# Kernel optimization log

Hardware: AMD Instinct MI355X
Metric: run time of the kernel (lower is better)

Reference implementation:

```python
import jax, jax.numpy as jnp
import numpy as np

B, I, H, N_STEPS = 256, 1024, 1024, 128


def setup_inputs() -> dict:
    key = jax.random.key(0)
    ks = jax.random.split(key, 12)
    s_ih = 1.0 / np.sqrt(H)
    u = lambda k, shp: jax.random.uniform(k, shp, jnp.float32, -s_ih, s_ih)
    return {
        "x": jax.random.normal(ks[0], (B, 1, I), jnp.float32),
        "n": N_STEPS,
        "w_ih_f": u(ks[1], (3 * H, I)),
        "w_hh_f": u(ks[2], (3 * H, H)),
        "b_ih_f": u(ks[3], (3 * H,)),
        "b_hh_f": u(ks[4], (3 * H,)),
        "w_ih_b": u(ks[5], (3 * H, I)),
        "w_hh_b": u(ks[6], (3 * H, H)),
        "b_ih_b": u(ks[7], (3 * H,)),
        "b_hh_b": u(ks[8], (3 * H,)),
        "w_out": u(ks[9], (1, 2 * H)),
        "b_out": u(ks[10], (1,)),
    }


def _gru_step(h, gi, w_hh, b_hh):
    # gi: precomputed input gates (B, 3H); h: (B, H)
    gh = h @ w_hh.T + b_hh
    gi_r, gi_z, gi_n = jnp.split(gi, 3, axis=-1)
    gh_r, gh_z, gh_n = jnp.split(gh, 3, axis=-1)
    r = jax.nn.sigmoid(gi_r + gh_r)
    z = jax.nn.sigmoid(gi_z + gh_z)
    ng = jnp.tanh(gi_n + r * gh_n)
    return (1.0 - z) * ng + z * h


def reference(x, n, w_ih_f, w_hh_f, b_ih_f, b_hh_f,
              w_ih_b, w_hh_b, b_ih_b, b_hh_b, w_out, b_out):
    x0 = x[:, 0, :]  # (B, I); cur_x never changes in the original loop
    # input-side gates are constant across steps (same x fed each time)
    gi_f = x0 @ w_ih_f.T + b_ih_f  # (B, 3H)
    gi_b = x0 @ w_ih_b.T + b_ih_b
    h0 = jnp.zeros((x.shape[0], w_hh_f.shape[1]), x.dtype)

    def step(carry, _):
        hf, hb = carry
        hf = _gru_step(hf, gi_f, w_hh_f, b_hh_f)
        hb = _gru_step(hb, gi_b, w_hh_b, b_hh_b)
        out = jnp.concatenate([hf, hb], axis=-1) @ w_out.T + b_out  # (B, 1)
        return (hf, hb), out

    _, outs = jax.lax.scan(step, (h0, h0), None, length=n)
    return jnp.transpose(outs, (1, 0, 2))  # (B, n, 1)
```

## Files before the change

kernel.cpp:

```cpp
#include <hip/hip_runtime.h>
#include <hip/hip_bf16.h>

typedef __attribute__((ext_vector_type(8))) __bf16 bf16x8;
typedef __attribute__((ext_vector_type(16))) float f32x16;
typedef __attribute__((ext_vector_type(4)))  float f32x4;

#define NB 256
#define HD 1024
#define G3 3072
#define NT 128

static const size_t OFF_WHH  = 0;
static const size_t OFF_WIH  = OFF_WHH + (size_t)2*G3*HD*2;
static const size_t OFF_X16  = OFF_WIH + (size_t)2*G3*HD*2;
static const size_t OFF_FLG  = OFF_X16 + (size_t)NB*HD*2;
static const size_t OFF_H16  = OFF_FLG + 65536;
static const size_t OFF_PART = OFF_H16 + (size_t)4*NB*HD*2;

__global__ __launch_bounds__(256) void prep_kernel(
    const float* __restrict__ x,    const float* __restrict__ wihf,
    const float* __restrict__ whhf, const float* __restrict__ wihb,
    const float* __restrict__ whhb, char* __restrict__ ws)
{
  size_t i = (size_t)blockIdx.x*256 + threadIdx.x;
  __hip_bfloat16* whh = (__hip_bfloat16*)(ws+OFF_WHH);
  __hip_bfloat16* wih = (__hip_bfloat16*)(ws+OFF_WIH);
  __hip_bfloat16* x16 = (__hip_bfloat16*)(ws+OFF_X16);
  __hip_bfloat16* h16 = (__hip_bfloat16*)(ws+OFF_H16);
  if (i < 16384) ((unsigned*)(ws+OFF_FLG))[i] = 0u;
  if (i < (size_t)G3*HD) {
    whh[i]                 = __float2bfloat16(whhf[i]);
    whh[(size_t)G3*HD + i] = __float2bfloat16(whhb[i]);
    wih[i]                 = __float2bfloat16(wihf[i]);
    wih[(size_t)G3*HD + i] = __float2bfloat16(wihb[i]);
  }
  if (i < (size_t)NB*HD)   x16[i] = __float2bfloat16(x[i]);
  if (i < (size_t)2*NB*HD) h16[i]  = __float2bfloat16(0.f);
}

__device__ inline f32x4 gload_cc(const void* p){
  f32x4 r;
  asm volatile("global_load_dwordx4 %0, %1, off sc0 sc1" : "=v"(r) : "v"(p) : "memory");
  return r;
}
__device__ inline void gstore_cc(void* p, f32x4 v){
  asm volatile("global_store_dwordx4 %0, %1, off sc0 sc1" :: "v"(p), "v"(v) : "memory");
}

__global__ __launch_bounds__(256,1)
void gru_persist(char* __restrict__ ws,
                 const float* __restrict__ bihf, const float* __restrict__ bhhf,
                 const float* __restrict__ bihb, const float* __restrict__ bhhb,
                 const float* __restrict__ wout)
{
  const int bid = blockIdx.x;
  const int g8  = bid & 7;
  const int d   = g8 >> 2;
  const int rt  = g8 & 3;
  const int jt  = bid >> 3;
  const int tid = threadIdx.x;
  const int q   = tid >> 6;
  const int l   = tid & 63;
  const int lrow = l & 31;
  const int lh   = l >> 5;
  const int erow = l & 15;
  const int ec   = l >> 4;
  const int r0 = rt*64, j0 = jt*32;

  const __hip_bfloat16* Wih = (const __hip_bfloat16*)(ws+OFF_WIH) + (size_t)d*G3*HD;
  const __hip_bfloat16* Whh = (const __hip_bfloat16*)(ws+OFF_WHH) + (size_t)d*G3*HD;
  const __hip_bfloat16* X16 = (const __hip_bfloat16*)(ws+OFF_X16);
  __hip_bfloat16* H16 = (__hip_bfloat16*)(ws+OFF_H16);
  unsigned* flg = (unsigned*)(ws+OFF_FLG);
  float* part = (float*)(ws+OFF_PART);

  __shared__ float red[4][64][100];

  const int kbase = (q*32 + lh)*8;

  bf16x8 B[3][16];
  auto loadB = [&](const __hip_bfloat16* Wsrc){
    #pragma unroll
    for (int g=0; g<3; ++g){
      const __hip_bfloat16* p0 = Wsrc + (size_t)(g*1024 + j0 + lrow)*HD + kbase;
      #pragma unroll
      for (int ks=0; ks<16; ++ks) B[g][ks] = *(const bf16x8*)(p0 + ks*16);
    }
  };

  f32x16 acc[2][3];
  auto gemm_cc = [&](const __hip_bfloat16* Asrc){
    #pragma unroll
    for (int mi=0;mi<2;++mi)
      #pragma unroll
      for (int g=0;g<3;++g)
        #pragma unroll
        for (int e=0;e<16;++e) acc[mi][g][e] = 0.f;
    const __hip_bfloat16* pa0 = Asrc + (size_t)(r0 + lrow)*HD + kbase;
    const __hip_bfloat16* pa1 = pa0 + 32*HD;
    f32x4 A0a[4], A0b[4], A1a[4], A1b[4];
    #pragma unroll
    for (int ks=0; ks<4; ++ks){ A0a[ks]=gload_cc(pa0+ks*16);      A1a[ks]=gload_cc(pa1+ks*16); }
    #pragma unroll
    for (int ks=0; ks<4; ++ks){ A0b[ks]=gload_cc(pa0+(4+ks)*16);  A1b[ks]=gload_cc(pa1+(4+ks)*16); }

    asm volatile("s_waitcnt vmcnt(8)" ::: "memory");
    __builtin_amdgcn_sched_barrier(0);
    #pragma unroll
    for (int ks=0; ks<4; ++ks){
      bf16x8 a0 = __builtin_bit_cast(bf16x8, A0a[ks]);
      bf16x8 a1 = __builtin_bit_cast(bf16x8, A1a[ks]);
      #pragma unroll
      for (int g=0; g<3; ++g){
        acc[0][g] = __builtin_amdgcn_mfma_f32_32x32x16_bf16(a0, B[g][ks], acc[0][g],0,0,0);
        acc[1][g] = __builtin_amdgcn_mfma_f32_32x32x16_bf16(a1, B[g][ks], acc[1][g],0,0,0);
      }
    }
    #pragma unroll
    for (int ks=0; ks<4; ++ks){ A0a[ks]=gload_cc(pa0+(8+ks)*16);  A1a[ks]=gload_cc(pa1+(8+ks)*16); }

    asm volatile("s_waitcnt vmcnt(8)" ::: "memory");
    __builtin_amdgcn_sched_barrier(0);
    #pragma unroll
    for (int ks=0; ks<4; ++ks){
      bf16x8 a0 = __builtin_bit_cast(bf16x8, A0b[ks]);
      bf16x8 a1 = __builtin_bit_cast(bf16x8, A1b[ks]);
      #pragma unroll
      for (int g=0; g<3; ++g){
        acc[0][g] = __builtin_amdgcn_mfma_f32_32x32x16_bf16(a0, B[g][4+ks], acc[0][g],0,0,0);
        acc[1][g] = __builtin_amdgcn_mfma_f32_32x32x16_bf16(a1, B[g][4+ks], acc[1][g],0,0,0);
      }
    }
    #pragma unroll
    for (int ks=0; ks<4; ++ks){ A0b[ks]=gload_cc(pa0+(12+ks)*16); A1b[ks]=gload_cc(pa1+(12+ks)*16); }

    asm volatile("s_waitcnt vmcnt(8)" ::: "memory");
    __builtin_amdgcn_sched_barrier(0);
    #pragma unroll
    for (int ks=0; ks<4; ++ks){
      bf16x8 a0 = __builtin_bit_cast(bf16x8, A0a[ks]);
      bf16x8 a1 = __builtin_bit_cast(bf16x8, A1a[ks]);
      #pragma unroll
      for (int g=0; g<3; ++g){
        acc[0][g] = __builtin_amdgcn_mfma_f32_32x32x16_bf16(a0, B[g][8+ks], acc[0][g],0,0,0);
        acc[1][g] = __builtin_amdgcn_mfma_f32_32x32x16_bf16(a1, B[g][8+ks], acc[1][g],0,0,0);
      }
    }

    asm volatile("s_waitcnt vmcnt(0)" ::: "memory");
    __builtin_amdgcn_sched_barrier(0);
    #pragma unroll
    for (int ks=0; ks<4; ++ks){
      bf16x8 a0 = __builtin_bit_cast(bf16x8, A0b[ks]);
      bf16x8 a1 = __builtin_bit_cast(bf16x8, A1b[ks]);
      #pragma unroll
      for (int g=0; g<3; ++g){
        acc[0][g] = __builtin_amdgcn_mfma_f32_32x32x16_bf16(a0, B[g][12+ks], acc[0][g],0,0,0);
        acc[1][g] = __builtin_amdgcn_mfma_f32_32x32x16_bf16(a1, B[g][12+ks], acc[1][g],0,0,0);
      }
    }
  };

  float val[3][8];
  auto reduce = [&](){
    #pragma unroll
    for (int mi=0;mi<2;++mi)
      #pragma unroll
      for (int g=0;g<3;++g)
        #pragma unroll
        for (int e=0;e<16;++e){
          int rl = mi*32 + (e&3) + 8*(e>>2) + 4*lh;
          red[q][rl][g*32 + lrow] = acc[mi][g][e];
        }
    __syncthreads();
    #pragma unroll
    for (int g=0; g<3; ++g){
      #pragma unroll
      for (int c=0;c<8;++c) val[g][c] = 0.f;
      #pragma unroll
      for (int qq=0; qq<4; ++qq){
        const float* base = &red[qq][q*16+erow][g*32 + ec*8];
        float4 v0 = *(const float4*)base;
        float4 v1 = *(const float4*)(base+4);
        val[g][0]+=v0.x; val[g][1]+=v0.y; val[g][2]+=v0.z; val[g][3]+=v0.w;
        val[g][4]+=v1.x; val[g][5]+=v1.y; val[g][6]+=v1.z; val[g][7]+=v1.w;
      }
    }
    __syncthreads();
  };

  loadB(Wih);
  gemm_cc(X16);
  reduce();
  const float* bih = d ? bihb : bihf;
  const float* bhh = d ? bhhb : bhhf;
  const int cg = j0 + ec*8;
  float gir[8], giz[8], gin[8], bhn[8], wo8[8], h[8];
  #pragma unroll
  for (int c=0;c<8;++c){
    gir[c] = val[0][c] + bih[cg+c]      + bhh[cg+c];
    giz[c] = val[1][c] + bih[1024+cg+c] + bhh[1024+cg+c];
    gin[c] = val[2][c] + bih[2048+cg+c];
    bhn[c] = bhh[2048+cg+c];
    wo8[c] = wout[d*HD + cg + c];
    h[c]   = 0.f;
  }

  loadB(Whh);
  const int myrow = r0 + q*16 + erow;
  const size_t hplane = (size_t)2*NB*HD;

  for (int t=0; t<NT; ++t){
    if (t){
      const unsigned tgt = (unsigned)t;
      unsigned* fp = flg + (size_t)(g8*32 + q*8 + (l & 7))*32;
      for(;;){
        unsigned v = (l < 8) ? __hip_atomic_load(fp, __ATOMIC_RELAXED, __HIP_MEMORY_SCOPE_AGENT) : tgt;
        if (__all((int)(v >= tgt))) break;
        __builtin_amdgcn_s_sleep(1);
      }
    }

    const __hip_bfloat16* hs = H16 + (size_t)(t&1)*hplane + (size_t)d*NB*HD;
    gemm_cc(hs);
    reduce();
    bf16x8 hv;
    float pp = 0.f;
    #pragma unroll
    for (int c=0;c<8;++c){
      float rr = 1.f/(1.f+__expf(-(gir[c]+val[0][c])));
      float zz = 1.f/(1.f+__expf(-(giz[c]+val[1][c])));
      float ar = gin[c] + rr*(val[2][c]+bhn[c]);
      float ng = 1.f - 2.f/(1.f + __expf(2.f*ar));
      h[c] = (1.f-zz)*ng + zz*h[c];
      hv[c] = (__bf16)h[c];
      pp += h[c]*wo8[c];
    }
    __hip_bfloat16* hd = H16 + (size_t)((t+1)&1)*hplane + (size_t)d*NB*HD;
    gstore_cc(hd + (size_t)myrow*HD + cg, __builtin_bit_cast(f32x4, hv));
    pp += __shfl_xor(pp, 16, 64);
    pp += __shfl_xor(pp, 32, 64);
    if (l < 16) part[((size_t)myrow*NT + t)*64 + d*32 + jt] = pp;

    asm volatile("s_waitcnt vmcnt(0)" ::: "memory");
    __syncthreads();
    if (t+1 < NT && tid == 0) atomicAdd(flg + (size_t)(g8*32 + jt)*32, 1u);
  }
}

__global__ __launch_bounds__(256) void finalize_kernel(
    const char* __restrict__ ws, const float* __restrict__ bout,
    float* __restrict__ out)
{
  int widx = blockIdx.x*4 + (threadIdx.x>>6);
  int lane = threadIdx.x & 63;
  const float* part = (const float*)(ws+OFF_PART);
  float v = part[(size_t)widx*64 + lane];
  #pragma unroll
  for (int m=1;m<64;m<<=1) v += __shfl_xor(v, m, 64);
  if (lane==0) out[widx] = v + bout[0];
}

extern "C" void kernel_launch(void* const* d_in, const int* in_sizes, int n_in,
                              void* d_out, int out_size, void* d_ws, size_t ws_size,
                              hipStream_t stream)
{
  const float* x    = (const float*)d_in[0];
  const float* wihf = (const float*)d_in[2];
  const float* whhf = (const float*)d_in[3];
  const float* bihf = (const float*)d_in[4];
  const float* bhhf = (const float*)d_in[5];
  const float* wihb = (const float*)d_in[6];
  const float* whhb = (const float*)d_in[7];
  const float* bihb = (const float*)d_in[8];
  const float* bhhb = (const float*)d_in[9];
  const float* wout = (const float*)d_in[10];
  const float* bout = (const float*)d_in[11];
  char* ws = (char*)d_ws;
  float* out = (float*)d_out;

  prep_kernel<<<12288, 256, 0, stream>>>(x, wihf, whhf, wihb, whhb, ws);
  gru_persist<<<256, 256, 0, stream>>>(ws, bihf, bhhf, bihb, bhhb, wout);
  finalize_kernel<<<8192, 256, 0, stream>>>(ws, bout, out);
}
```

Before: 1.059 ms.

## Use L2-scoped h loads/stores when all communicating blocks share an XCC

Each block records its XCC id at runtime, and the blocks that exchange hidden state (same g8 group) check whether they all sit on the same XCC. If they do, the per-step h exchange uses loads and stores with L2-level coherence instead of system-coherent sc0 sc1 accesses, aiming to cut the latency of the recurrent GEMM's operand fetch. Otherwise it falls back to the old path. It adds a one-time global census with spinning, and the fast path relies on block-to-XCC placement, which the hardware may not provide.

```diff
diff --git a/kernel.cpp b/kernel.cpp
--- a/kernel.cpp
+++ b/kernel.cpp
@@ -14,6 +14,8 @@
 static const size_t OFF_WIH  = OFF_WHH + (size_t)2*G3*HD*2;
 static const size_t OFF_X16  = OFF_WIH + (size_t)2*G3*HD*2;
 static const size_t OFF_FLG  = OFF_X16 + (size_t)NB*HD*2;
+static const size_t OFF_XTAB = OFF_FLG + 32768;
+static const size_t OFF_XCNT = OFF_XTAB + 1024;
 static const size_t OFF_H16  = OFF_FLG + 65536;
 static const size_t OFF_PART = OFF_H16 + (size_t)4*NB*HD*2;
 
@@ -46,6 +48,75 @@
 __device__ inline void gstore_cc(void* p, f32x4 v){
   asm volatile("global_store_dwordx4 %0, %1, off sc0 sc1" :: "v"(p), "v"(v) : "memory");
 }
+__device__ inline f32x4 gload_l2(const void* p){
+  f32x4 r;
+  asm volatile("global_load_dwordx4 %0, %1, off sc0" : "=v"(r) : "v"(p) : "memory");
+  return r;
+}
+__device__ inline void gstore_l2(void* p, f32x4 v){
+  asm volatile("global_store_dwordx4 %0, %1, off" :: "v"(p), "v"(v) : "memory");
+}
+__device__ inline unsigned gload_u32_cc(const void* p){
+  unsigned r;
+  asm volatile("global_load_dword %0, %1, off sc0 sc1" : "=v"(r) : "v"(p) : "memory");
+  return r;
+}
+__device__ inline void gstore_u32_cc(void* p, unsigned v){
+  asm volatile("global_store_dword %0, %1, off sc0 sc1" :: "v"(p), "v"(v) : "memory");
+}
+
+#define GEMM_BODY(ASRC, LOADH) { \
+    _Pragma("unroll") for (int mi=0;mi<2;++mi) \
+      _Pragma("unroll") for (int g=0;g<3;++g) \
+        _Pragma("unroll") for (int e=0;e<16;++e) acc[mi][g][e] = 0.f; \
+    const __hip_bfloat16* pa0 = (ASRC) + (size_t)(r0 + lrow)*HD + kbase; \
+    const __hip_bfloat16* pa1 = pa0 + 32*HD; \
+    f32x4 A0a[4], A0b[4], A1a[4], A1b[4]; \
+    _Pragma("unroll") for (int ks=0; ks<4; ++ks){ A0a[ks]=LOADH(pa0+ks*16);      A1a[ks]=LOADH(pa1+ks*16); } \
+    _Pragma("unroll") for (int ks=0; ks<4; ++ks){ A0b[ks]=LOADH(pa0+(4+ks)*16);  A1b[ks]=LOADH(pa1+(4+ks)*16); } \
+    asm volatile("s_waitcnt vmcnt(8)" ::: "memory"); \
+    __builtin_amdgcn_sched_barrier(0); \
+    _Pragma("unroll") for (int ks=0; ks<4; ++ks){ \
+      bf16x8 a0 = __builtin_bit_cast(bf16x8, A0a[ks]); \
+      bf16x8 a1 = __builtin_bit_cast(bf16x8, A1a[ks]); \
+      _Pragma("unroll") for (int g=0; g<3; ++g){ \
+        acc[0][g] = __builtin_amdgcn_mfma_f32_32x32x16_bf16(a0, B[g][ks], acc[0][g],0,0,0); \
+        acc[1][g] = __builtin_amdgcn_mfma_f32_32x32x16_bf16(a1, B[g][ks], acc[1][g],0,0,0); \
+      } \
+    } \
+    _Pragma("unroll") for (int ks=0; ks<4; ++ks){ A0a[ks]=LOADH(pa0+(8+ks)*16);  A1a[ks]=LOADH(pa1+(8+ks)*16); } \
+    asm volatile("s_waitcnt vmcnt(8)" ::: "memory"); \
+    __builtin_amdgcn_sched_barrier(0); \
+    _Pragma("unroll") for (int ks=0; ks<4; ++ks){ \
+      bf16x8 a0 = __builtin_bit_cast(bf16x8, A0b[ks]); \
+      bf16x8 a1 = __builtin_bit_cast(bf16x8, A1b[ks]); \
+      _Pragma("unroll") for (int g=0; g<3; ++g){ \
+        acc[0][g] = __builtin_amdgcn_mfma_f32_32x32x16_bf16(a0, B[g][4+ks], acc[0][g],0,0,0); \
+        acc[1][g] = __builtin_amdgcn_mfma_f32_32x32x16_bf16(a1, B[g][4+ks], acc[1][g],0,0,0); \
+      } \
+    } \
+    _Pragma("unroll") for (int ks=0; ks<4; ++ks){ A0b[ks]=LOADH(pa0+(12+ks)*16); A1b[ks]=LOADH(pa1+(12+ks)*16); } \
+    asm volatile("s_waitcnt vmcnt(8)" ::: "memory"); \
+    __builtin_amdgcn_sched_barrier(0); \
+    _Pragma("unroll") for (int ks=0; ks<4; ++ks){ \
+      bf16x8 a0 = __builtin_bit_cast(bf16x8, A0a[ks]); \
+      bf16x8 a1 = __builtin_bit_cast(bf16x8, A1a[ks]); \
+      _Pragma("unroll") for (int g=0; g<3; ++g){ \
+        acc[0][g] = __builtin_amdgcn_mfma_f32_32x32x16_bf16(a0, B[g][8+ks], acc[0][g],0,0,0); \
+        acc[1][g] = __builtin_amdgcn_mfma_f32_32x32x16_bf16(a1, B[g][8+ks], acc[1][g],0,0,0); \
+      } \
+    } \
+    asm volatile("s_waitcnt vmcnt(0)" ::: "memory"); \
+    __builtin_amdgcn_sched_barrier(0); \
+    _Pragma("unroll") for (int ks=0; ks<4; ++ks){ \
+      bf16x8 a0 = __builtin_bit_cast(bf16x8, A0b[ks]); \
+      bf16x8 a1 = __builtin_bit_cast(bf16x8, A1b[ks]); \
+      _Pragma("unroll") for (int g=0; g<3; ++g){ \
+        acc[0][g] = __builtin_amdgcn_mfma_f32_32x32x16_bf16(a0, B[g][12+ks], acc[0][g],0,0,0); \
+        acc[1][g] = __builtin_amdgcn_mfma_f32_32x32x16_bf16(a1, B[g][12+ks], acc[1][g],0,0,0); \
+      } \
+    } \
+  }
 
 __global__ __launch_bounds__(256,1)
 void gru_persist(char* __restrict__ ws,
@@ -71,10 +142,13 @@
   const __hip_bfloat16* Whh = (const __hip_bfloat16*)(ws+OFF_WHH) + (size_t)d*G3*HD;
   const __hip_bfloat16* X16 = (const __hip_bfloat16*)(ws+OFF_X16);
   __hip_bfloat16* H16 = (__hip_bfloat16*)(ws+OFF_H16);
-  unsigned* flg = (unsigned*)(ws+OFF_FLG);
+  unsigned* flg  = (unsigned*)(ws+OFF_FLG);
+  unsigned* xtab = (unsigned*)(ws+OFF_XTAB);
+  unsigned* xcnt = (unsigned*)(ws+OFF_XCNT);
   float* part = (float*)(ws+OFF_PART);
 
   __shared__ float red[4][64][100];
+  __shared__ unsigned oksh;
 
   const int kbase = (q*32 + lh)*8;
 
@@ -89,78 +163,6 @@
   };
 
   f32x16 acc[2][3];
-  auto gemm_cc = [&](const __hip_bfloat16* Asrc){
-    #pragma unroll
-    for (int mi=0;mi<2;++mi)
-      #pragma unroll
-      for (int g=0;g<3;++g)
-        #pragma unroll
-        for (int e=0;e<16;++e) acc[mi][g][e] = 0.f;
-    const __hip_bfloat16* pa0 = Asrc + (size_t)(r0 + lrow)*HD + kbase;
-    const __hip_bfloat16* pa1 = pa0 + 32*HD;
-    f32x4 A0a[4], A0b[4], A1a[4], A1b[4];
-    #pragma unroll
-    for (int ks=0; ks<4; ++ks){ A0a[ks]=gload_cc(pa0+ks*16);      A1a[ks]=gload_cc(pa1+ks*16); }
-    #pragma unroll
-    for (int ks=0; ks<4; ++ks){ A0b[ks]=gload_cc(pa0+(4+ks)*16);  A1b[ks]=gload_cc(pa1+(4+ks)*16); }
-
-    asm volatile("s_waitcnt vmcnt(8)" ::: "memory");
-    __builtin_amdgcn_sched_barrier(0);
-    #pragma unroll
-    for (int ks=0; ks<4; ++ks){
-      bf16x8 a0 = __builtin_bit_cast(bf16x8, A0a[ks]);
-      bf16x8 a1 = __builtin_bit_cast(bf16x8, A1a[ks]);
-      #pragma unroll
-      for (int g=0; g<3; ++g){
-        acc[0][g] = __builtin_amdgcn_mfma_f32_32x32x16_bf16(a0, B[g][ks], acc[0][g],0,0,0);
-        acc[1][g] = __builtin_amdgcn_mfma_f32_32x32x16_bf16(a1, B[g][ks], acc[1][g],0,0,0);
-      }
-    }
-    #pragma unroll
-    for (int ks=0; ks<4; ++ks){ A0a[ks]=gload_cc(pa0+(8+ks)*16);  A1a[ks]=gload_cc(pa1+(8+ks)*16); }
-
-    asm volatile("s_waitcnt vmcnt(8)" ::: "memory");
-    __builtin_amdgcn_sched_barrier(0);
-    #pragma unroll
-    for (int ks=0; ks<4; ++ks){
-      bf16x8 a0 = __builtin_bit_cast(bf16x8, A0b[ks]);
-      bf16x8 a1 = __builtin_bit_cast(bf16x8, A1b[ks]);
-      #pragma unroll
-      for (int g=0; g<3; ++g){
-        acc[0][g] = __builtin_amdgcn_mfma_f32_32x32x16_bf16(a0, B[g][4+ks], acc[0][g],0,0,0);
-        acc[1][g] = __builtin_amdgcn_mfma_f32_32x32x16_bf16(a1, B[g][4+ks], acc[1][g],0,0,0);
-      }
-    }
-    #pragma unroll
-    for (int ks=0; ks<4; ++ks){ A0b[ks]=gload_cc(pa0+(12+ks)*16); A1b[ks]=gload_cc(pa1+(12+ks)*16); }
-
-    asm volatile("s_waitcnt vmcnt(8)" ::: "memory");
-    __builtin_amdgcn_sched_barrier(0);
-    #pragma unroll
-    for (int ks=0; ks<4; ++ks){
-      bf16x8 a0 = __builtin_bit_cast(bf16x8, A0a[ks]);
-      bf16x8 a1 = __builtin_bit_cast(bf16x8, A1a[ks]);
-      #pragma unroll
-      for (int g=0; g<3; ++g){
-        acc[0][g] = __builtin_amdgcn_mfma_f32_32x32x16_bf16(a0, B[g][8+ks], acc[0][g],0,0,0);
-        acc[1][g] = __builtin_amdgcn_mfma_f32_32x32x16_bf16(a1, B[g][8+ks], acc[1][g],0,0,0);
-      }
-    }
-
-    asm volatile("s_waitcnt vmcnt(0)" ::: "memory");
-    __builtin_amdgcn_sched_barrier(0);
-    #pragma unroll
-    for (int ks=0; ks<4; ++ks){
-      bf16x8 a0 = __builtin_bit_cast(bf16x8, A0b[ks]);
-      bf16x8 a1 = __builtin_bit_cast(bf16x8, A1b[ks]);
-      #pragma unroll
-      for (int g=0; g<3; ++g){
-        acc[0][g] = __builtin_amdgcn_mfma_f32_32x32x16_bf16(a0, B[g][12+ks], acc[0][g],0,0,0);
-        acc[1][g] = __builtin_amdgcn_mfma_f32_32x32x16_bf16(a1, B[g][12+ks], acc[1][g],0,0,0);
-      }
-    }
-  };
-
   float val[3][8];
   auto reduce = [&](){
     #pragma unroll
@@ -189,8 +191,16 @@
     __syncthreads();
   };
 
+  unsigned xcc;
+  asm volatile("s_getreg_b32 %0, hwreg(HW_REG_XCC_ID)" : "=s"(xcc));
+  if (tid == 0){
+    gstore_u32_cc(xtab + bid, xcc);
+    asm volatile("s_waitcnt vmcnt(0)" ::: "memory");
+    atomicAdd(xcnt, 1u);
+  }
+
   loadB(Wih);
-  gemm_cc(X16);
+  GEMM_BODY(X16, gload_l2);
   reduce();
   const float* bih = d ? bihb : bihf;
   const float* bhh = d ? bhhb : bhhf;
@@ -205,8 +215,23 @@
     wo8[c] = wout[d*HD + cg + c];
     h[c]   = 0.f;
   }
-
   loadB(Whh);
+
+  if (tid == 0){
+    while (__hip_atomic_load(xcnt, __ATOMIC_RELAXED, __HIP_MEMORY_SCOPE_AGENT) < 256u)
+      __builtin_amdgcn_s_sleep(2);
+    unsigned all_ok = 1u, ref = gload_u32_cc(xtab + g8);
+    asm volatile("s_waitcnt vmcnt(0)" ::: "memory");
+    for (int i=1; i<32; ++i){
+      unsigned v = gload_u32_cc(xtab + g8 + i*8);
+      asm volatile("s_waitcnt vmcnt(0)" ::: "memory");
+      if (v != ref) all_ok = 0u;
+    }
+    oksh = all_ok;
+  }
+  __syncthreads();
+  const bool okf = (oksh != 0u);
+
   const int myrow = r0 + q*16 + erow;
   const size_t hplane = (size_t)2*NB*HD;
 
@@ -222,8 +247,9 @@
     }
 
     const __hip_bfloat16* hs = H16 + (size_t)(t&1)*hplane + (size_t)d*NB*HD;
-    gemm_cc(hs);
+    if (okf) { GEMM_BODY(hs, gload_l2); } else { GEMM_BODY(hs, gload_cc); }
     reduce();
+
     bf16x8 hv;
     float pp = 0.f;
     #pragma unroll
@@ -237,7 +263,9 @@
       pp += h[c]*wo8[c];
     }
     __hip_bfloat16* hd = H16 + (size_t)((t+1)&1)*hplane + (size_t)d*NB*HD;
-    gstore_cc(hd + (size_t)myrow*HD + cg, __builtin_bit_cast(f32x4, hv));
+    f32x4 hvv = __builtin_bit_cast(f32x4, hv);
+    if (okf) gstore_l2(hd + (size_t)myrow*HD + cg, hvv);
+    else     gstore_cc(hd + (size_t)myrow*HD + cg, hvv);
     pp += __shfl_xor(pp, 16, 64);
     pp += __shfl_xor(pp, 32, 64);
     if (l < 16) part[((size_t)myrow*NT + t)*64 + d*32 + jt] = pp;
```

Result: faster. 1.017 ms (-4.0%).
